# Performance work log

Measured on AMD Instinct MI355X. Metric: run time of the kernel, lower is better.

Reference implementation:

```python
import jax, jax.numpy as jnp
import numpy as np

CLASS_COUNT = 21
THRESHOLD = 0.5
ALPHA = 0.25
GAMMA = 2.0
VARIANCE = (0.1, 0.2)

B, A, N_OBJ = 32, 24576, 16


def point_form(boxes):
    # center form (cx, cy, w, h) -> point form (xmin, ymin, xmax, ymax)
    return jnp.concatenate([boxes[:, :2] - boxes[:, 2:] / 2,
                            boxes[:, :2] + boxes[:, 2:] / 2], axis=1)


def jaccard(truths, priors):
    # truths [N,4], priors [A,4] both in point form -> IoU [N, A]
    lt = jnp.maximum(truths[:, None, :2], priors[None, :, :2])
    rb = jnp.minimum(truths[:, None, 2:], priors[None, :, 2:])
    wh = jnp.clip(rb - lt, 0.0, None)
    inter = wh[..., 0] * wh[..., 1]
    area_t = ((truths[:, 2] - truths[:, 0]) * (truths[:, 3] - truths[:, 1]))[:, None]
    area_p = ((priors[:, 2] - priors[:, 0]) * (priors[:, 3] - priors[:, 1]))[None, :]
    return inter / (area_t + area_p - inter)


def match_one(labels, truths, anchors):
    # labels [N] int, truths [N,4] point form, anchors [A,4] center form
    overlaps = jaccard(truths, point_form(anchors))           # [N, A]
    best_prior_idx = jnp.argmax(overlaps, axis=1)             # [N]
    best_truth_overlap = jnp.max(overlaps, axis=0)            # [A]
    best_truth_idx = jnp.argmax(overlaps, axis=0)             # [A]
    # ensure every gt matches its best prior
    best_truth_overlap = best_truth_overlap.at[best_prior_idx].set(2.0)
    best_truth_idx = best_truth_idx.at[best_prior_idx].set(jnp.arange(truths.shape[0]))
    matches = truths[best_truth_idx]                          # [A, 4]
    conf = jnp.where(best_truth_overlap < THRESHOLD, 0, labels[best_truth_idx])
    # encode with variances
    g_cxcy = ((matches[:, :2] + matches[:, 2:]) * 0.5 - anchors[:, :2]) / (VARIANCE[0] * anchors[:, 2:])
    g_wh = jnp.log((matches[:, 2:] - matches[:, :2]) / anchors[:, 2:]) / VARIANCE[1]
    return conf, jnp.concatenate([g_cxcy, g_wh], axis=1)


def setup_inputs() -> dict:
    key = jax.random.key(0)
    k1, k2, k3, k4, k5, k6, k7 = jax.random.split(key, 7)
    class_preds = jax.random.normal(k1, (B, A, CLASS_COUNT), dtype=jnp.float32)
    loc_preds = jax.random.normal(k2, (B, A, 4), dtype=jnp.float32)
    # ground-truth boxes: random valid point-form boxes in [0,1]
    ctr = jax.random.uniform(k3, (B, N_OBJ, 2), minval=0.2, maxval=0.8)
    wh = jax.random.uniform(k4, (B, N_OBJ, 2), minval=0.05, maxval=0.3)
    loc_targets = jnp.clip(jnp.concatenate([ctr - wh / 2, ctr + wh / 2], axis=-1), 0.0, 1.0)
    class_targets = jax.random.randint(k5, (B, N_OBJ), 1, CLASS_COUNT)
    # anchors in center form
    a_ctr = jax.random.uniform(k6, (A, 2), minval=0.05, maxval=0.95)
    a_wh = jax.random.uniform(k7, (A, 2), minval=0.05, maxval=0.4)
    anchors = jnp.concatenate([a_ctr, a_wh], axis=1)
    return {"class_preds": class_preds, "loc_preds": loc_preds,
            "loc_targets": loc_targets, "anchors": anchors,
            "class_targets": class_targets}


def reference(class_preds, loc_preds, loc_targets, anchors, class_targets):
    conf, loc_t = jax.vmap(match_one, in_axes=(0, 0, None))(class_targets, loc_targets, anchors)
    pos = conf > 0                                            # [B, A]
    num_matched = jnp.sum(pos).astype(jnp.float32)
    # smooth L1 over positive anchors (sum reduction, beta=1)
    d = loc_preds - loc_t
    ad = jnp.abs(d)
    sl1 = jnp.where(ad < 1.0, 0.5 * d * d, ad - 0.5)
    loc_loss = jnp.sum(sl1 * pos[..., None].astype(sl1.dtype))
    # focal loss (drop background column 0)
    cp = class_preds.reshape(-1, CLASS_COUNT)[:, 1:]          # [B*A, C-1]
    t = jax.nn.one_hot(conf.reshape(-1), CLASS_COUNT, dtype=cp.dtype)[:, 1:]
    p = jax.nn.sigmoid(cp)
    pt = jnp.where(t > 0, p, 1.0 - p)
    w = (1.0 - pt) ** GAMMA
    w = jnp.where(t > 0, ALPHA * w, (1.0 - ALPHA) * w)
    # stable binary cross entropy with logits, weighted, sum reduction
    bce = jnp.maximum(cp, 0.0) - cp * t + jnp.log1p(jnp.exp(-jnp.abs(cp)))
    class_loss = jnp.sum(w * bce)
    class_loss = class_loss / num_matched
    loc_loss = loc_loss / num_matched
    return jnp.stack([class_loss, loc_loss, class_loss + loc_loss])
```

## Files before the change

kernel.cpp:

```cpp
#include <hip/hip_runtime.h>

#define A_COUNT 24576
#define B_COUNT 32
#define NOBJ 16
#define C_COUNT 21

#define NCH 32
#define CHUNK (A_COUNT / NCH)
#define NBLK (NCH * B_COUNT)
#define TOTAL4 (B_COUNT * A_COUNT * C_COUNT / 4)

#define WS_BPP 0
#define WS_LOCP 131072
#define WS_CLSP 135168
#define WS_POSP 139264
#define WS_DLOC 143360
#define WS_DCLS 143488
#define WS_DPOS 143616

__device__ __forceinline__ unsigned long long pack_key(float iou, int a) {
    unsigned int ib = __float_as_uint(iou);
    return ((unsigned long long)ib << 32) | (unsigned long long)(0xFFFFFFFFu - (unsigned int)a);
}

__device__ __forceinline__ float iou_pf(float tx0, float ty0, float tx1, float ty1, float at,
                                        float x0, float y0, float x1, float y1, float ap) {
    float lx = fmaxf(tx0, x0), ly = fmaxf(ty0, y0);
    float rx = fminf(tx1, x1), ry = fminf(ty1, y1);
    float w = fmaxf(rx - lx, 0.0f), h = fmaxf(ry - ly, 0.0f);
    float inter = w * h;
    return inter / (at + ap - inter);
}

__device__ __forceinline__ float sl1(float d) {
    float ad = fabsf(d);
    return (ad < 1.0f) ? 0.5f * d * d : ad - 0.5f;
}

__device__ __forceinline__ float loc_term(float4 t, float4 an, float4 lp) {
    float gx = ((t.x + t.z) * 0.5f - an.x) / (0.1f * an.z);
    float gy = ((t.y + t.w) * 0.5f - an.y) / (0.1f * an.w);
    float gw = __logf((t.z - t.x) / an.z) * 5.0f;
    float gh = __logf((t.w - t.y) / an.w) * 5.0f;
    return sl1(lp.x - gx) + sl1(lp.y - gy) + sl1(lp.z - gw) + sl1(lp.w - gh);
}

__device__ __forceinline__ float corr_term(float x) {
    float E = __expf(x);
    float den = 1.0f + E;
    float s = __builtin_amdgcn_rcpf(den);
    float p = E * s;
    float L = __logf(den);
    return 0.25f * s * s * (L - x) - 0.75f * p * p * L;
}

__global__ __launch_bounds__(256, 4) void k_main(const float* __restrict__ cls,
                                                 const float4* __restrict__ locp,
                                                 const float4* __restrict__ anchors,
                                                 const float4* __restrict__ truths,
                                                 const int* __restrict__ labels,
                                                 unsigned long long* __restrict__ bp_partial,
                                                 float* __restrict__ loc_partial,
                                                 float* __restrict__ cls_partial,
                                                 unsigned int* __restrict__ pos_partial) {
    const int ch = blockIdx.x;
    const int b = blockIdx.y;
    const int tid = threadIdx.x;
    __shared__ float4 s_t[NOBJ];
    __shared__ float s_area[NOBJ];
    __shared__ int s_lab[NOBJ];
    __shared__ unsigned long long s_keys[8][256];
    if (tid < NOBJ) {
        float4 t = truths[b * NOBJ + tid];
        s_t[tid] = t;
        s_area[tid] = (t.z - t.x) * (t.w - t.y);
        s_lab[tid] = labels[b * NOBJ + tid];
    }
    __syncthreads();
    const int a0 = ch * CHUNK + tid;
    const int a1 = a0 + 256;
    const int a2 = a0 + 512;
    float4 an0 = anchors[a0];
    float4 an1 = anchors[a1];
    float4 an2 = anchors[a2];
    float p0x0 = an0.x - an0.z * 0.5f, p0y0 = an0.y - an0.w * 0.5f;
    float p0x1 = an0.x + an0.z * 0.5f, p0y1 = an0.y + an0.w * 0.5f;
    float ap0 = (p0x1 - p0x0) * (p0y1 - p0y0);
    float p1x0 = an1.x - an1.z * 0.5f, p1y0 = an1.y - an1.w * 0.5f;
    float p1x1 = an1.x + an1.z * 0.5f, p1y1 = an1.y + an1.w * 0.5f;
    float ap1 = (p1x1 - p1x0) * (p1y1 - p1y0);
    float p2x0 = an2.x - an2.z * 0.5f, p2y0 = an2.y - an2.w * 0.5f;
    float p2x1 = an2.x + an2.z * 0.5f, p2y1 = an2.y + an2.w * 0.5f;
    float ap2 = (p2x1 - p2x0) * (p2y1 - p2y0);
    float best0 = -1.0f, best1 = -1.0f, best2 = -1.0f;
    int idx0 = 0, idx1 = 0, idx2 = 0;
#pragma unroll
    for (int half = 0; half < 2; ++half) {
#pragma unroll
        for (int n = 0; n < 8; ++n) {
            const int nt = half * 8 + n;
            float4 t = s_t[nt];
            float at = s_area[nt];
            float iou0 = iou_pf(t.x, t.y, t.z, t.w, at, p0x0, p0y0, p0x1, p0y1, ap0);
            float iou1 = iou_pf(t.x, t.y, t.z, t.w, at, p1x0, p1y0, p1x1, p1y1, ap1);
            float iou2 = iou_pf(t.x, t.y, t.z, t.w, at, p2x0, p2y0, p2x1, p2y1, ap2);
            if (iou0 > best0) { best0 = iou0; idx0 = nt; }
            if (iou1 > best1) { best1 = iou1; idx1 = nt; }
            if (iou2 > best2) { best2 = iou2; idx2 = nt; }
            unsigned long long key = pack_key(iou0, a0);
            unsigned long long k1 = pack_key(iou1, a1);
            key = (k1 > key) ? k1 : key;
            unsigned long long k2 = pack_key(iou2, a2);
            key = (k2 > key) ? k2 : key;
            s_keys[n][tid] = key;
        }
        __syncthreads();
        if (tid < 128) {
            const int g = tid >> 4, l = tid & 15;
            unsigned long long k = s_keys[g][l];
#pragma unroll
            for (int kk = 1; kk < 16; ++kk) {
                unsigned long long v = s_keys[g][l + 16 * kk];
                k = (v > k) ? v : k;
            }
#pragma unroll
            for (int s = 8; s >= 1; s >>= 1) {
                unsigned long long o = __shfl_xor(k, s);
                k = (o > k) ? o : k;
            }
            if (l == 0) bp_partial[(b * NOBJ + half * 8 + g) * NCH + ch] = k;
        }
        __syncthreads();
    }
    float loc_l = 0.0f, cls_acc = 0.0f;
    unsigned int pos = 0;
    if (!(best0 < 0.5f)) {
        pos++;
        loc_l += loc_term(s_t[idx0], an0, locp[(size_t)b * A_COUNT + a0]);
        cls_acc += corr_term(cls[((size_t)b * A_COUNT + a0) * C_COUNT + s_lab[idx0]]);
    }
    if (!(best1 < 0.5f)) {
        pos++;
        loc_l += loc_term(s_t[idx1], an1, locp[(size_t)b * A_COUNT + a1]);
        cls_acc += corr_term(cls[((size_t)b * A_COUNT + a1) * C_COUNT + s_lab[idx1]]);
    }
    if (!(best2 < 0.5f)) {
        pos++;
        loc_l += loc_term(s_t[idx2], an2, locp[(size_t)b * A_COUNT + a2]);
        cls_acc += corr_term(cls[((size_t)b * A_COUNT + a2) * C_COUNT + s_lab[idx2]]);
    }

    const int bid = b * NCH + ch;
    {
        const float4* cls4 = (const float4*)cls;
        int i = bid * 256 + tid;
        unsigned int f = (unsigned int)i * 4u;
        unsigned int dq = f / 21u;
        int r = (int)(f - dq * 21u);
        const int stride = NBLK * 256;
        for (; i < TOTAL4; i += stride) {
            float4 x4 = cls4[i];
            float xs[4] = {x4.x, x4.y, x4.z, x4.w};
#pragma unroll
            for (int j = 0; j < 4; ++j) {
                int rr = r + j;
                float x = xs[j];
                float E = __expf(x);
                float den = 1.0f + E;
                float s = __builtin_amdgcn_rcpf(den);
                float p = E * s;
                float L = __logf(den);
                float v = p * p * L;
                float m = (rr == 0 || rr == 21) ? 0.0f : 0.75f;
                cls_acc = fmaf(v, m, cls_acc);
            }
            r += 4; if (r >= 21) r -= 21;
        }
    }

#pragma unroll
    for (int s = 32; s >= 1; s >>= 1) {
        loc_l += __shfl_xor(loc_l, s);
        cls_acc += __shfl_xor(cls_acc, s);
        pos += __shfl_xor(pos, s);
    }
    __shared__ float s_ll[4], s_cl[4];
    __shared__ unsigned int s_pp[4];
    if ((tid & 63) == 0) {
        s_ll[tid >> 6] = loc_l;
        s_cl[tid >> 6] = cls_acc;
        s_pp[tid >> 6] = pos;
    }
    __syncthreads();
    if (tid == 0) {
        loc_partial[bid] = s_ll[0] + s_ll[1] + s_ll[2] + s_ll[3];
        cls_partial[bid] = s_cl[0] + s_cl[1] + s_cl[2] + s_cl[3];
        pos_partial[bid] = s_pp[0] + s_pp[1] + s_pp[2] + s_pp[3];
    }
}

__global__ __launch_bounds__(256) void k_fix(const float* __restrict__ cls,
                                             const float4* __restrict__ locp,
                                             const float4* __restrict__ anchors,
                                             const float4* __restrict__ truths,
                                             const int* __restrict__ labels,
                                             const unsigned long long* __restrict__ bp_partial,
                                             float* __restrict__ dloc,
                                             float* __restrict__ dcls,
                                             int* __restrict__ dpos) {
    const int b = blockIdx.x;
    const int tid = threadIdx.x;
    __shared__ int s_bp[NOBJ];
    {
        const int g = tid >> 4, l = tid & 15;
        const unsigned long long* pp = &bp_partial[(size_t)(b * NOBJ + g) * NCH];
        unsigned long long k = pp[l];
        unsigned long long v = pp[l + 16];
        k = (v > k) ? v : k;
#pragma unroll
        for (int s = 8; s >= 1; s >>= 1) {
            unsigned long long o = __shfl_xor(k, s);
            k = (o > k) ? o : k;
        }
        if (l == 0) {
            unsigned int ia = 0xFFFFFFFFu - (unsigned int)(k & 0xFFFFFFFFull);
            s_bp[g] = (ia >= A_COUNT) ? -1 : (int)ia;
        }
    }
    __syncthreads();
    float d_loc = 0.0f, d_cls = 0.0f;
    int d_pos = 0;
    if (tid < NOBJ) {
        const int n = tid;
        const int q = s_bp[n];
        bool winner = (q >= 0);
        for (int n2 = n + 1; n2 < NOBJ; ++n2)
            if (s_bp[n2] == q) winner = false;
        if (winner) {
            float4 an = anchors[q];
            float px0 = an.x - an.z * 0.5f, py0 = an.y - an.w * 0.5f;
            float px1 = an.x + an.z * 0.5f, py1 = an.y + an.w * 0.5f;
            float ap = (px1 - px0) * (py1 - py0);
            float best = -1.0f;
            int idx = 0;
            for (int n2 = 0; n2 < NOBJ; ++n2) {
                float4 t = truths[b * NOBJ + n2];
                float at = (t.z - t.x) * (t.w - t.y);
                float iou = iou_pf(t.x, t.y, t.z, t.w, at, px0, py0, px1, py1, ap);
                if (iou > best) { best = iou; idx = n2; }
            }
            float4 lp = locp[(size_t)b * A_COUNT + q];
            if (!(best < 0.5f)) {
                d_pos -= 1;
                d_loc -= loc_term(truths[b * NOBJ + idx], an, lp);
                d_cls -= corr_term(cls[((size_t)b * A_COUNT + q) * C_COUNT + labels[b * NOBJ + idx]]);
            }
            d_pos += 1;
            d_loc += loc_term(truths[b * NOBJ + n], an, lp);
            d_cls += corr_term(cls[((size_t)b * A_COUNT + q) * C_COUNT + labels[b * NOBJ + n]]);
        }
    }
    if (tid < 64) {
#pragma unroll
        for (int s = 8; s >= 1; s >>= 1) {
            d_loc += __shfl_xor(d_loc, s);
            d_cls += __shfl_xor(d_cls, s);
            d_pos += __shfl_xor(d_pos, s);
        }
        if (tid == 0) {
            dloc[b] = d_loc;
            dcls[b] = d_cls;
            dpos[b] = d_pos;
        }
    }
}

__global__ __launch_bounds__(256) void k_final(const float* __restrict__ loc_partial,
                                               const float* __restrict__ cls_partial,
                                               const unsigned int* __restrict__ pos_partial,
                                               const float* __restrict__ dloc,
                                               const float* __restrict__ dcls,
                                               const int* __restrict__ dpos,
                                               float* __restrict__ out) {
    const int tid = threadIdx.x;
    double loc = 0.0, clsv = 0.0;
    int pos = 0;
    for (int i = tid; i < NBLK; i += 256) {
        loc += (double)loc_partial[i];
        clsv += (double)cls_partial[i];
        pos += (int)pos_partial[i];
    }
    if (tid < B_COUNT) {
        loc += (double)dloc[tid];
        clsv += (double)dcls[tid];
        pos += dpos[tid];
    }
#pragma unroll
    for (int s = 32; s >= 1; s >>= 1) {
        loc += __shfl_xor(loc, s);
        clsv += __shfl_xor(clsv, s);
        pos += __shfl_xor(pos, s);
    }
    __shared__ double s_l[4], s_c[4];
    __shared__ int s_p[4];
    if ((tid & 63) == 0) {
        s_l[tid >> 6] = loc;
        s_c[tid >> 6] = clsv;
        s_p[tid >> 6] = pos;
    }
    __syncthreads();
    if (tid == 0) {
        double L = s_l[0] + s_l[1] + s_l[2] + s_l[3];
        double Cv = s_c[0] + s_c[1] + s_c[2] + s_c[3];
        float nm = (float)(s_p[0] + s_p[1] + s_p[2] + s_p[3]);
        float cf = (float)Cv / nm;
        float lf = (float)L / nm;
        out[0] = cf;
        out[1] = lf;
        out[2] = cf + lf;
    }
}

extern "C" void kernel_launch(void* const* d_in, const int* in_sizes, int n_in,
                              void* d_out, int out_size, void* d_ws, size_t ws_size,
                              hipStream_t stream) {
    const float* cls = (const float*)d_in[0];
    const float4* locp = (const float4*)d_in[1];
    const float4* truths = (const float4*)d_in[2];
    const float4* anchors = (const float4*)d_in[3];
    const int* labels = (const int*)d_in[4];

    char* ws = (char*)d_ws;
    unsigned long long* bp_partial = (unsigned long long*)(ws + WS_BPP);
    float* loc_partial = (float*)(ws + WS_LOCP);
    float* cls_partial = (float*)(ws + WS_CLSP);
    unsigned int* pos_partial = (unsigned int*)(ws + WS_POSP);
    float* dloc = (float*)(ws + WS_DLOC);
    float* dcls = (float*)(ws + WS_DCLS);
    int* dpos = (int*)(ws + WS_DPOS);

    k_main<<<dim3(NCH, B_COUNT), 256, 0, stream>>>(cls, locp, anchors, truths, labels,
                                                   bp_partial, loc_partial, cls_partial, pos_partial);
    k_fix<<<B_COUNT, 256, 0, stream>>>(cls, locp, anchors, truths, labels, bp_partial,
                                       dloc, dcls, dpos);
    k_final<<<1, 256, 0, stream>>>(loc_partial, cls_partial, pos_partial, dloc, dcls, dpos,
                                   (float*)d_out);
}
```

Baseline: 44.60 us.

## Fuse fix-up and final reduction into main kernel via last-block atomic counter

```diff
diff --git a/kernel.cpp b/kernel.cpp
--- a/kernel.cpp
+++ b/kernel.cpp
@@ -8,15 +8,15 @@
 #define NCH 32
 #define CHUNK (A_COUNT / NCH)
 #define NBLK (NCH * B_COUNT)
+#define NROWS (B_COUNT * NOBJ)
 #define TOTAL4 (B_COUNT * A_COUNT * C_COUNT / 4)
+#define STRIDE4 (NBLK * 256)
 
 #define WS_BPP 0
 #define WS_LOCP 131072
 #define WS_CLSP 135168
 #define WS_POSP 139264
-#define WS_DLOC 143360
-#define WS_DCLS 143488
-#define WS_DPOS 143616
+#define WS_CNT 143360
 
 __device__ __forceinline__ unsigned long long pack_key(float iou, int a) {
     unsigned int ib = __float_as_uint(iou);
@@ -54,15 +54,27 @@
     return 0.25f * s * s * (L - x) - 0.75f * p * p * L;
 }
 
-__global__ __launch_bounds__(256, 4) void k_main(const float* __restrict__ cls,
-                                                 const float4* __restrict__ locp,
-                                                 const float4* __restrict__ anchors,
-                                                 const float4* __restrict__ truths,
-                                                 const int* __restrict__ labels,
-                                                 unsigned long long* __restrict__ bp_partial,
-                                                 float* __restrict__ loc_partial,
-                                                 float* __restrict__ cls_partial,
-                                                 unsigned int* __restrict__ pos_partial) {
+#define FOC(xv, rr, acc) {                                   \
+    float E_ = __expf(xv);                                   \
+    float den_ = 1.0f + E_;                                  \
+    float s_ = __builtin_amdgcn_rcpf(den_);                  \
+    float p_ = E_ * s_;                                      \
+    float L_ = __logf(den_);                                 \
+    float v_ = p_ * p_ * L_;                                 \
+    float m_ = ((rr) == 0 || (rr) == 21) ? 0.0f : 0.75f;     \
+    acc = fmaf(v_, m_, acc); }
+
+__global__ __launch_bounds__(256, 4) void k_all(const float* __restrict__ cls,
+                                                const float4* __restrict__ locp,
+                                                const float4* __restrict__ anchors,
+                                                const float4* __restrict__ truths,
+                                                const int* __restrict__ labels,
+                                                unsigned long long* __restrict__ bp_partial,
+                                                float* __restrict__ loc_partial,
+                                                float* __restrict__ cls_partial,
+                                                unsigned int* __restrict__ pos_partial,
+                                                unsigned int* __restrict__ counter,
+                                                float* __restrict__ out) {
     const int ch = blockIdx.x;
     const int b = blockIdx.y;
     const int tid = threadIdx.x;
@@ -157,25 +169,23 @@
         unsigned int f = (unsigned int)i * 4u;
         unsigned int dq = f / 21u;
         int r = (int)(f - dq * 21u);
-        const int stride = NBLK * 256;
-        for (; i < TOTAL4; i += stride) {
-            float4 x4 = cls4[i];
-            float xs[4] = {x4.x, x4.y, x4.z, x4.w};
-#pragma unroll
-            for (int j = 0; j < 4; ++j) {
-                int rr = r + j;
-                float x = xs[j];
-                float E = __expf(x);
-                float den = 1.0f + E;
-                float s = __builtin_amdgcn_rcpf(den);
-                float p = E * s;
-                float L = __logf(den);
-                float v = p * p * L;
-                float m = (rr == 0 || rr == 21) ? 0.0f : 0.75f;
-                cls_acc = fmaf(v, m, cls_acc);
-            }
-            r += 4; if (r >= 21) r -= 21;
-        }
+        float acc0 = 0.0f, acc1 = 0.0f, acc2 = 0.0f, acc3 = 0.0f;
+        for (; i + STRIDE4 < TOTAL4; i += 2 * STRIDE4) {
+            float4 xA = cls4[i];
+            float4 xB = cls4[i + STRIDE4];
+            int rB = r + 4;
+            FOC(xA.x, r + 0, acc0); FOC(xA.y, r + 1, acc1);
+            FOC(xA.z, r + 2, acc2); FOC(xA.w, r + 3, acc3);
+            FOC(xB.x, rB + 0, acc0); FOC(xB.y, rB + 1, acc1);
+            FOC(xB.z, rB + 2, acc2); FOC(xB.w, rB + 3, acc3);
+            r += 8; if (r >= 21) r -= 21;
+        }
+        if (i < TOTAL4) {
+            float4 xA = cls4[i];
+            FOC(xA.x, r + 0, acc0); FOC(xA.y, r + 1, acc1);
+            FOC(xA.z, r + 2, acc2); FOC(xA.w, r + 3, acc3);
+        }
+        cls_acc += (acc0 + acc1) + (acc2 + acc3);
     }
 
 #pragma unroll
@@ -197,116 +207,91 @@
         cls_partial[bid] = s_cl[0] + s_cl[1] + s_cl[2] + s_cl[3];
         pos_partial[bid] = s_pp[0] + s_pp[1] + s_pp[2] + s_pp[3];
     }
-}
-
-__global__ __launch_bounds__(256) void k_fix(const float* __restrict__ cls,
-                                             const float4* __restrict__ locp,
-                                             const float4* __restrict__ anchors,
-                                             const float4* __restrict__ truths,
-                                             const int* __restrict__ labels,
-                                             const unsigned long long* __restrict__ bp_partial,
-                                             float* __restrict__ dloc,
-                                             float* __restrict__ dcls,
-                                             int* __restrict__ dpos) {
-    const int b = blockIdx.x;
-    const int tid = threadIdx.x;
-    __shared__ int s_bp[NOBJ];
+
+    __syncthreads();
+    __shared__ unsigned int s_last;
+    if (tid == 0) {
+        __threadfence();
+        unsigned int old = atomicAdd(counter, 1u);
+        s_last = (old == NBLK - 1) ? 1u : 0u;
+    }
+    __syncthreads();
+    if (s_last == 0u) return;
+    __threadfence();
+
+    __shared__ int s_bp[NROWS];
     {
         const int g = tid >> 4, l = tid & 15;
-        const unsigned long long* pp = &bp_partial[(size_t)(b * NOBJ + g) * NCH];
-        unsigned long long k = pp[l];
-        unsigned long long v = pp[l + 16];
-        k = (v > k) ? v : k;
-#pragma unroll
-        for (int s = 8; s >= 1; s >>= 1) {
-            unsigned long long o = __shfl_xor(k, s);
-            k = (o > k) ? o : k;
-        }
-        if (l == 0) {
-            unsigned int ia = 0xFFFFFFFFu - (unsigned int)(k & 0xFFFFFFFFull);
-            s_bp[g] = (ia >= A_COUNT) ? -1 : (int)ia;
-        }
-    }
-    __syncthreads();
+        for (int base = 0; base < NROWS; base += 16) {
+            const int row = base + g;
+            const unsigned long long* pp = &bp_partial[(size_t)row * NCH];
+            unsigned long long k = pp[l];
+            unsigned long long v = pp[l + 16];
+            k = (v > k) ? v : k;
+#pragma unroll
+            for (int s = 8; s >= 1; s >>= 1) {
+                unsigned long long o = __shfl_xor(k, s);
+                k = (o > k) ? o : k;
+            }
+            if (l == 0) {
+                unsigned int ia = 0xFFFFFFFFu - (unsigned int)(k & 0xFFFFFFFFull);
+                s_bp[row] = (ia >= A_COUNT) ? -1 : (int)ia;
+            }
+        }
+    }
+    __syncthreads();
+
     float d_loc = 0.0f, d_cls = 0.0f;
     int d_pos = 0;
-    if (tid < NOBJ) {
-        const int n = tid;
-        const int q = s_bp[n];
+    for (int pr = tid; pr < NROWS; pr += 256) {
+        const int b2 = pr >> 4, n = pr & 15;
+        const int q = s_bp[pr];
         bool winner = (q >= 0);
         for (int n2 = n + 1; n2 < NOBJ; ++n2)
-            if (s_bp[n2] == q) winner = false;
-        if (winner) {
-            float4 an = anchors[q];
-            float px0 = an.x - an.z * 0.5f, py0 = an.y - an.w * 0.5f;
-            float px1 = an.x + an.z * 0.5f, py1 = an.y + an.w * 0.5f;
-            float ap = (px1 - px0) * (py1 - py0);
-            float best = -1.0f;
-            int idx = 0;
-            for (int n2 = 0; n2 < NOBJ; ++n2) {
-                float4 t = truths[b * NOBJ + n2];
-                float at = (t.z - t.x) * (t.w - t.y);
-                float iou = iou_pf(t.x, t.y, t.z, t.w, at, px0, py0, px1, py1, ap);
-                if (iou > best) { best = iou; idx = n2; }
-            }
-            float4 lp = locp[(size_t)b * A_COUNT + q];
-            if (!(best < 0.5f)) {
-                d_pos -= 1;
-                d_loc -= loc_term(truths[b * NOBJ + idx], an, lp);
-                d_cls -= corr_term(cls[((size_t)b * A_COUNT + q) * C_COUNT + labels[b * NOBJ + idx]]);
-            }
-            d_pos += 1;
-            d_loc += loc_term(truths[b * NOBJ + n], an, lp);
-            d_cls += corr_term(cls[((size_t)b * A_COUNT + q) * C_COUNT + labels[b * NOBJ + n]]);
-        }
-    }
-    if (tid < 64) {
-#pragma unroll
-        for (int s = 8; s >= 1; s >>= 1) {
-            d_loc += __shfl_xor(d_loc, s);
-            d_cls += __shfl_xor(d_cls, s);
-            d_pos += __shfl_xor(d_pos, s);
-        }
-        if (tid == 0) {
-            dloc[b] = d_loc;
-            dcls[b] = d_cls;
-            dpos[b] = d_pos;
-        }
-    }
-}
-
-__global__ __launch_bounds__(256) void k_final(const float* __restrict__ loc_partial,
-                                               const float* __restrict__ cls_partial,
-                                               const unsigned int* __restrict__ pos_partial,
-                                               const float* __restrict__ dloc,
-                                               const float* __restrict__ dcls,
-                                               const int* __restrict__ dpos,
-                                               float* __restrict__ out) {
-    const int tid = threadIdx.x;
-    double loc = 0.0, clsv = 0.0;
-    int pos = 0;
-    for (int i = tid; i < NBLK; i += 256) {
-        loc += (double)loc_partial[i];
-        clsv += (double)cls_partial[i];
-        pos += (int)pos_partial[i];
-    }
-    if (tid < B_COUNT) {
-        loc += (double)dloc[tid];
-        clsv += (double)dcls[tid];
-        pos += dpos[tid];
+            if (s_bp[(b2 << 4) | n2] == q) winner = false;
+        if (!winner) continue;
+        float4 an = anchors[q];
+        float px0 = an.x - an.z * 0.5f, py0 = an.y - an.w * 0.5f;
+        float px1 = an.x + an.z * 0.5f, py1 = an.y + an.w * 0.5f;
+        float ap = (px1 - px0) * (py1 - py0);
+        float best = -1.0f;
+        int idx = 0;
+        for (int n2 = 0; n2 < NOBJ; ++n2) {
+            float4 t = truths[b2 * NOBJ + n2];
+            float at = (t.z - t.x) * (t.w - t.y);
+            float iou = iou_pf(t.x, t.y, t.z, t.w, at, px0, py0, px1, py1, ap);
+            if (iou > best) { best = iou; idx = n2; }
+        }
+        float4 lp = locp[(size_t)b2 * A_COUNT + q];
+        if (!(best < 0.5f)) {
+            d_pos -= 1;
+            d_loc -= loc_term(truths[b2 * NOBJ + idx], an, lp);
+            d_cls -= corr_term(cls[((size_t)b2 * A_COUNT + q) * C_COUNT + labels[b2 * NOBJ + idx]]);
+        }
+        d_pos += 1;
+        d_loc += loc_term(truths[b2 * NOBJ + n], an, lp);
+        d_cls += corr_term(cls[((size_t)b2 * A_COUNT + q) * C_COUNT + labels[b2 * NOBJ + n]]);
+    }
+
+    double loc = (double)d_loc, clsv = (double)d_cls;
+    int posx = d_pos;
+    for (int k2 = tid; k2 < NBLK; k2 += 256) {
+        loc += (double)loc_partial[k2];
+        clsv += (double)cls_partial[k2];
+        posx += (int)pos_partial[k2];
     }
 #pragma unroll
     for (int s = 32; s >= 1; s >>= 1) {
         loc += __shfl_xor(loc, s);
         clsv += __shfl_xor(clsv, s);
-        pos += __shfl_xor(pos, s);
+        posx += __shfl_xor(posx, s);
     }
     __shared__ double s_l[4], s_c[4];
     __shared__ int s_p[4];
     if ((tid & 63) == 0) {
         s_l[tid >> 6] = loc;
         s_c[tid >> 6] = clsv;
-        s_p[tid >> 6] = pos;
+        s_p[tid >> 6] = posx;
     }
     __syncthreads();
     if (tid == 0) {
@@ -335,14 +320,10 @@
     float* loc_partial = (float*)(ws + WS_LOCP);
     float* cls_partial = (float*)(ws + WS_CLSP);
     unsigned int* pos_partial = (unsigned int*)(ws + WS_POSP);
-    float* dloc = (float*)(ws + WS_DLOC);
-    float* dcls = (float*)(ws + WS_DCLS);
-    int* dpos = (int*)(ws + WS_DPOS);
-
-    k_main<<<dim3(NCH, B_COUNT), 256, 0, stream>>>(cls, locp, anchors, truths, labels,
-                                                   bp_partial, loc_partial, cls_partial, pos_partial);
-    k_fix<<<B_COUNT, 256, 0, stream>>>(cls, locp, anchors, truths, labels, bp_partial,
-                                       dloc, dcls, dpos);
-    k_final<<<1, 256, 0, stream>>>(loc_partial, cls_partial, pos_partial, dloc, dcls, dpos,
-                                   (float*)d_out);
-}
+    unsigned int* counter = (unsigned int*)(ws + WS_CNT);
+
+    hipMemsetAsync(counter, 0, 4, stream);
+    k_all<<<dim3(NCH, B_COUNT), 256, 0, stream>>>(cls, locp, anchors, truths, labels,
+                                                  bp_partial, loc_partial, cls_partial,
+                                                  pos_partial, counter, (float*)d_out);
+}
```

Result: slower. 87.52 us (+96.3%).
